# Kernel tuning notes

Measured on AMD Instinct MI355X. Metric: run time of the kernel, lower is better.

Reference implementation:

```python
import jax, jax.numpy as jnp
import numpy as np

N_USERS, N_ITEMS, P, F = 100000, 200000, 8, 64
B, S = 4096, 200

def setup_inputs() -> dict:
    key = jax.random.key(0)
    k1, k2, k3, k4 = jax.random.split(key, 4)
    user = jax.random.randint(k1, (B,), 0, N_USERS)
    items = jax.random.randint(k2, (B, S), 0, N_ITEMS)
    # xavier_normal init: std = sqrt(2/(fan_in+fan_out)) per torch semantics on last two dims
    std_u = np.sqrt(2.0 / (P + F))
    std_i = np.sqrt(2.0 / (N_ITEMS + F))
    user_factors = jax.random.normal(k3, (N_USERS, P, F), dtype=jnp.float32) * std_u
    item_factors = jax.random.normal(k4, (N_ITEMS, F), dtype=jnp.float32) * std_i
    return {"user": user, "items": items, "user_factors": user_factors, "item_factors": item_factors}

def reference(user, items, user_factors, item_factors):
    u = user_factors[user]          # [B, P, F]
    v = item_factors[items]         # [B, S, F]
    r = jnp.einsum('bsf,bpf->bsp', v, u)            # [B, S, P]
    attentive_scores = jax.nn.softmax(r, axis=-1)   # softmax over personas
    attentive_user = jnp.einsum('bpf,bsp->bsf', u, attentive_scores)  # [B, S, F]
    pred = jnp.einsum('bsf,bsf->bs', attentive_user, v)               # [B, S]
    return (pred, attentive_scores)
```

## Files before the change

### kernel.cpp

```cpp
#include <hip/hip_runtime.h>

#define NB 4096
#define NS 200
#define NP 8
#define NF 64
#define CHUNKS (NF / 4)

__global__ __launch_bounds__(256) void cf_kernel(
    const int*   __restrict__ user,
    const int*   __restrict__ items,
    const float* __restrict__ user_factors,
    const float* __restrict__ item_factors,
    float* __restrict__ out_pred,
    float* __restrict__ out_scores)
{
    __shared__ float u_lds[NF * NP];
    __shared__ int   idx_lds[NS];
    __shared__ float v_lds[NS * NF];

    const int b   = blockIdx.x;
    const int tid = threadIdx.x;

    {
        const int uid = user[b];
        const float2* ub = (const float2*)(user_factors + (size_t)uid * (NP * NF));
        float2 w = ub[tid];
        int e0 = tid * 2;
        u_lds[(e0 & 63) * NP + (e0 >> 6)] = w.x;
        int e1 = e0 + 1;
        u_lds[(e1 & 63) * NP + (e1 >> 6)] = w.y;
    }
    if (tid < NS) idx_lds[tid] = items[b * NS + tid];
    __syncthreads();

    for (int q = tid; q < NS * CHUNKS; q += 256) {
        int row  = q >> 4;
        int k    = q & 15;
        int gidx = idx_lds[row];
        float4 val = ((const float4*)(item_factors + (size_t)gidx * NF))[k];
        int pos = k ^ (row & 15);
        ((float4*)&v_lds[row * NF])[pos] = val;
    }
    __syncthreads();

    const int s = tid;
    if (s >= NS) return;

    const int sx = s & 15;
    const float4* vrow = (const float4*)&v_lds[s * NF];

    float r[NP];
    #pragma unroll
    for (int p = 0; p < NP; ++p) r[p] = 0.f;

    #pragma unroll
    for (int c = 0; c < NF / 8; ++c) {
        float4 v0 = vrow[(2 * c)     ^ sx];
        float4 v1 = vrow[(2 * c + 1) ^ sx];
        float vf[8] = {v0.x, v0.y, v0.z, v0.w, v1.x, v1.y, v1.z, v1.w};
        #pragma unroll
        for (int j = 0; j < 8; ++j) {
            const float4* up = (const float4*)&u_lds[(c * 8 + j) * NP];
            float4 a  = up[0];
            float4 bb = up[1];
            float vv = vf[j];
            r[0] += vv * a.x;  r[1] += vv * a.y;  r[2] += vv * a.z;  r[3] += vv * a.w;
            r[4] += vv * bb.x; r[5] += vv * bb.y; r[6] += vv * bb.z; r[7] += vv * bb.w;
        }
    }

    float m = r[0];
    #pragma unroll
    for (int p = 1; p < NP; ++p) m = fmaxf(m, r[p]);
    float e[NP];
    float sum = 0.f;
    #pragma unroll
    for (int p = 0; p < NP; ++p) { e[p] = __expf(r[p] - m); sum += e[p]; }
    float inv = 1.f / sum;

    float sc[NP];
    float pred = 0.f;
    #pragma unroll
    for (int p = 0; p < NP; ++p) {
        sc[p] = e[p] * inv;
        pred += sc[p] * r[p];
    }

    out_pred[b * NS + s] = pred;
    float4* op = (float4*)(out_scores + (size_t)(b * NS + s) * NP);
    op[0] = make_float4(sc[0], sc[1], sc[2], sc[3]);
    op[1] = make_float4(sc[4], sc[5], sc[6], sc[7]);
}

extern "C" void kernel_launch(void* const* d_in, const int* in_sizes, int n_in,
                              void* d_out, int out_size, void* d_ws, size_t ws_size,
                              hipStream_t stream) {
    const int*   user         = (const int*)d_in[0];
    const int*   items        = (const int*)d_in[1];
    const float* user_factors = (const float*)d_in[2];
    const float* item_factors = (const float*)d_in[3];

    float* out_pred   = (float*)d_out;
    float* out_scores = out_pred + (size_t)NB * NS;

    cf_kernel<<<NB, 256, 0, stream>>>(user, items, user_factors, item_factors,
                                      out_pred, out_scores);
}
```

Measured before the change: 343.8 us.

## Gather item rows directly into LDS with global_load_lds and drop index staging

Replaces the register-staged gather of item factor rows with the global_load_lds builtin, which writes 16-byte chunks straight into shared memory. Item indices are loaded per thread into registers instead of going through an LDS index array, which removes one barrier. The XOR swizzle moves from the destination side to the source side so the LDS layout stays the same. This is meant to cut VGPR traffic and let all gathers be issued up front. In exchange it relies on 16-byte direct-to-LDS load support and on the builtin's wave-contiguous LDS placement being correct.

```diff
diff --git a/kernel.cpp b/kernel.cpp
--- a/kernel.cpp
+++ b/kernel.cpp
@@ -5,6 +5,8 @@
 #define NP 8
 #define NF 64
 #define CHUNKS (NF / 4)
+#define NCHUNK (NS * CHUNKS)
+#define MAXIT ((NCHUNK + 255) / 256)
 
 __global__ __launch_bounds__(256) void cf_kernel(
     const int*   __restrict__ user,
@@ -15,32 +17,49 @@
     float* __restrict__ out_scores)
 {
     __shared__ float u_lds[NF * NP];
-    __shared__ int   idx_lds[NS];
     __shared__ float v_lds[NS * NF];
 
-    const int b   = blockIdx.x;
-    const int tid = threadIdx.x;
+    const int b    = blockIdx.x;
+    const int tid  = threadIdx.x;
+    const int wave = tid >> 6;
+    const int lane = tid & 63;
+
+    const int uid = user[b];
+    const float2 w = ((const float2*)(user_factors + (size_t)uid * (NP * NF)))[tid];
+
+    int gidx[MAXIT];
+    #pragma unroll
+    for (int i = 0; i < MAXIT; ++i) {
+        int qb = i * 256 + wave * 64;
+        if (qb < NCHUNK) {
+            int row = (qb + lane) >> 4;
+            gidx[i] = items[b * NS + row];
+        }
+    }
+
+    #pragma unroll
+    for (int i = 0; i < MAXIT; ++i) {
+        int qb = i * 256 + wave * 64;
+        if (qb < NCHUNK) {
+            int q   = qb + lane;
+            int row = q >> 4;
+            int kp  = q & 15;
+            int k   = kp ^ (row & 15);
+            const float* src = item_factors + (size_t)gidx[i] * NF + k * 4;
+            __builtin_amdgcn_global_load_lds(
+                (const __attribute__((address_space(1))) void*)src,
+                (__attribute__((address_space(3))) void*)&v_lds[qb * 4],
+                16, 0, 0);
+        }
+    }
 
     {
-        const int uid = user[b];
-        const float2* ub = (const float2*)(user_factors + (size_t)uid * (NP * NF));
-        float2 w = ub[tid];
         int e0 = tid * 2;
         u_lds[(e0 & 63) * NP + (e0 >> 6)] = w.x;
         int e1 = e0 + 1;
         u_lds[(e1 & 63) * NP + (e1 >> 6)] = w.y;
     }
-    if (tid < NS) idx_lds[tid] = items[b * NS + tid];
-    __syncthreads();
 
-    for (int q = tid; q < NS * CHUNKS; q += 256) {
-        int row  = q >> 4;
-        int k    = q & 15;
-        int gidx = idx_lds[row];
-        float4 val = ((const float4*)(item_factors + (size_t)gidx * NF))[k];
-        int pos = k ^ (row & 15);
-        ((float4*)&v_lds[row * NF])[pos] = val;
-    }
     __syncthreads();
 
     const int s = tid;
```

New measurement: 299.2 us. -13.0%, faster.
